# Kernel optimization log

Measured on AMD Instinct MI355X. Metric: run time of the kernel, lower is better.

The kernel has to match this reference:

```python
import jax, jax.numpy as jnp
import numpy as np

ALPHA = 0.25
GAMMA = 2.0
W_CLASS = W_BBOX = W_GIOU = W_MASK = W_DICE = W_PROJ = 1.0
EPS = 1e-8


def box_cxcywh_to_xyxy(b):
    cx, cy, w, h = jnp.split(b, 4, axis=-1)
    return jnp.concatenate([cx - 0.5 * w, cy - 0.5 * h, cx + 0.5 * w, cy + 0.5 * h], axis=-1)


def dice_coef(inputs, targets):
    # inputs: logits [N, D]; targets: binary [M, D]
    s = jax.nn.sigmoid(inputs)
    num = 2.0 * jnp.einsum('nd,md->nm', s, targets)
    den = s.sum(-1)[:, None] + targets.sum(-1)[None, :]
    return (num + 1.0) / (den + 1.0)  # [N, M]


def sigmoid_focal_coef(inputs, targets):
    # inputs: logits [N, D]; targets: binary [M, D] -> [N, M]
    x = inputs[:, None, :]
    t = targets[None, :, :]
    p = jax.nn.sigmoid(x)
    # BCE-with-logits, numerically stable
    ce = jnp.maximum(x, 0.0) - x * t + jnp.log1p(jnp.exp(-jnp.abs(x)))
    p_t = p * t + (1.0 - p) * (1.0 - t)
    alpha_t = ALPHA * t + (1.0 - ALPHA) * (1.0 - t)
    return (alpha_t * ce * (1.0 - p_t) ** GAMMA).mean(-1)


def giou_cost(src_xyxy, tgt_xyxy):
    # src [nf, nq, 4], tgt [nf, 1, 4] -> cost [nf, nq, 1]
    a1 = (src_xyxy[..., 2] - src_xyxy[..., 0]) * (src_xyxy[..., 3] - src_xyxy[..., 1])
    a2 = (tgt_xyxy[..., 2] - tgt_xyxy[..., 0]) * (tgt_xyxy[..., 3] - tgt_xyxy[..., 1])
    lt = jnp.maximum(src_xyxy[:, :, None, :2], tgt_xyxy[:, None, :, :2])
    rb = jnp.minimum(src_xyxy[:, :, None, 2:], tgt_xyxy[:, None, :, 2:])
    wh = jnp.clip(rb - lt, 0.0)
    inter = wh[..., 0] * wh[..., 1]
    union = a1[:, :, None] + a2[:, None, :] - inter
    iou = inter / union
    ltc = jnp.minimum(src_xyxy[:, :, None, :2], tgt_xyxy[:, None, :, :2])
    rbc = jnp.maximum(src_xyxy[:, :, None, 2:], tgt_xyxy[:, None, :, 2:])
    whc = jnp.clip(rbc - ltc, 0.0)
    areac = whc[..., 0] * whc[..., 1]
    giou = iou - (areac - union) / areac
    return -giou


def cost_matrix_one(logits, boxes, masks, tmask, tbox, tvalid):
    # logits [nf,nq,1], boxes [nf,nq,4], masks [nf,nq,H,W], tmask [nf,H,W], tbox [nf,4], tvalid [nf]
    p = jax.nn.sigmoid(logits[..., 0])  # [nf, nq]
    neg = (1.0 - ALPHA) * p ** GAMMA * (-jnp.log(1.0 - p + EPS))
    pos = ALPHA * (1.0 - p) ** GAMMA * (-jnp.log(p + EPS))
    w = (tvalid != 0).astype(p.dtype)  # valid-frame mask replaces python `continue`
    cost_class = (((pos - neg) * w[:, None]).sum(0) / w.sum())[:, None]  # [nq, 1]

    cost_bbox = jnp.abs(boxes[:, :, None, :] - tbox[:, None, None, :]).sum(-1).mean(0)  # [nq, 1]
    cost_giou = giou_cost(box_cxcywh_to_xyxy(boxes), box_cxcywh_to_xyxy(tbox[:, None, :])).mean(0)

    out_mask = jnp.transpose(masks, (1, 0, 2, 3))  # [nq, nf, H, W]
    nq = out_mask.shape[0]
    flat_src = out_mask.reshape(nq, -1)
    flat_tgt = tmask.reshape(1, -1)
    cost_mask = sigmoid_focal_coef(flat_src, flat_tgt)  # [nq, 1]
    cost_dice = -dice_coef(flat_src, flat_tgt)

    src_y = jnp.max(out_mask, axis=2, keepdims=True).reshape(nq, -1)  # [nq, nf*W]
    src_x = jnp.max(out_mask, axis=3, keepdims=True).reshape(nq, -1)  # [nq, nf*H]
    tgt_y = jnp.max(tmask[None], axis=2, keepdims=True).reshape(1, -1)
    tgt_x = jnp.max(tmask[None], axis=3, keepdims=True).reshape(1, -1)
    cost_proj = -0.5 * (dice_coef(src_y, tgt_y) + dice_coef(src_x, tgt_x))

    C = (W_CLASS * cost_class + W_BBOX * cost_bbox + W_GIOU * cost_giou
         + W_MASK * cost_mask + W_DICE * cost_dice + W_PROJ * cost_proj)
    return C  # [nq, 1]


def setup_inputs() -> dict:
    key = jax.random.key(0)
    k = jax.random.split(key, 6)
    bs, nf, nq, H, W = 2, 8, 300, 96, 96
    pred_logits = jax.random.normal(k[0], (bs, nf, nq, 1), dtype=jnp.float32)
    pred_boxes = jax.random.uniform(k[1], (bs, nf, nq, 4), dtype=jnp.float32)
    pred_masks = jax.random.normal(k[2], (bs, nf, nq, H, W), dtype=jnp.float32)
    target_masks = (jax.random.uniform(k[3], (bs, nf, H, W)) < 0.3).astype(jnp.float32)
    tgt_boxes = jax.random.uniform(k[4], (bs, nf, 4), dtype=jnp.float32)
    tgt_valid = jnp.ones((bs, nf), dtype=jnp.int32)
    valid_pad = jnp.zeros((bs, H, W), dtype=bool)
    return {"pred_logits": pred_logits, "pred_boxes": pred_boxes, "pred_masks": pred_masks,
            "target_masks": target_masks, "tgt_boxes": tgt_boxes, "tgt_valid": tgt_valid,
            "valid_pad": valid_pad}


def reference(pred_logits, pred_boxes, pred_masks, target_masks, tgt_boxes, tgt_valid, valid_pad):
    # zero out predictions over padded regions (masked_fill with valid[:, None, None])
    masks = jnp.where(valid_pad[:, None, None, :, :], 0.0, pred_masks)
    C = jax.vmap(cost_matrix_one)(pred_logits, pred_boxes, masks, target_masks, tgt_boxes, tgt_valid)
    src_ind = jnp.argmin(C, axis=1).astype(jnp.int64)  # [bs, 1]
    tgt_ind = jnp.zeros_like(src_ind)
    return C, src_ind, tgt_ind
```

## Files before the change

kernel.cpp:

```cpp
#include <hip/hip_runtime.h>
#include <math.h>

#define NF 8
#define NQ 300
#define HSZ 96
#define WSZ 96
#define HW 9216
#define DTOT 73728
#define NT 256
#define NTP 192
#define NBF 16

#define WS_TGTY 0
#define WS_TGTX 1536
#define WS_TSUM 3072
#define WS_YSUM 3088
#define WS_XSUM 3104
#define WS_TBITS 3200
#define WS_PBITS 7808
#define WS_PART  8448

__device__ __forceinline__ float sigmoid_fast(float x) {
    float e = __expf(-fabsf(x));
    float inv = __builtin_amdgcn_rcpf(1.f + e);
    return x >= 0.f ? inv : e * inv;
}

__global__ __launch_bounds__(NT)
void targets_kernel(const float* __restrict__ tm, const unsigned char* __restrict__ vpad,
                    float* __restrict__ ws) {
    int bf = blockIdx.x, t = threadIdx.x;
    int lane = t & 63, wv = t >> 6;
    __shared__ float tile[HSZ * 97];
    __shared__ float red[4][4];
    unsigned long long* tb64 = (unsigned long long*)(ws + WS_TBITS) + bf * 144;
    const float* base = tm + (size_t)bf * HW;
    float tsum = 0.f;
    #pragma unroll
    for (int it = 0; it < 36; ++it) {
        int e = it * NT + t;
        float v = base[e];
        tsum += v;
        unsigned long long bt = __ballot(v != 0.f);
        if (lane == 0) tb64[it * 4 + wv] = bt;
        tile[e + e / 96] = v;
    }
    if ((bf & 7) == 0) {
        int b = bf >> 3;
        unsigned long long* pb64 = (unsigned long long*)(ws + WS_PBITS) + b * 144;
        const unsigned char* pp = vpad + (size_t)b * HW;
        #pragma unroll
        for (int it = 0; it < 36; ++it) {
            int e = it * NT + t;
            unsigned long long bt = __ballot(pp[e] != 0);
            if (lane == 0) pb64[it * 4 + wv] = bt;
        }
    }
    __syncthreads();
    float ysum = 0.f, xsum = 0.f;
    if (t < 96) {
        float m = -INFINITY;
        #pragma unroll 8
        for (int h = 0; h < HSZ; ++h) m = fmaxf(m, tile[h * 97 + t]);
        ws[WS_TGTY + bf * 96 + t] = m;
        ysum = m;
    } else if (t < 192) {
        int hh = t - 96;
        float m = -INFINITY;
        #pragma unroll 8
        for (int w = 0; w < WSZ; ++w) m = fmaxf(m, tile[hh * 97 + w]);
        ws[WS_TGTX + bf * 96 + hh] = m;
        xsum = m;
    }
    float v0 = tsum, v1 = ysum, v2 = xsum;
    #pragma unroll
    for (int off = 32; off > 0; off >>= 1) {
        v0 += __shfl_down(v0, off, 64);
        v1 += __shfl_down(v1, off, 64);
        v2 += __shfl_down(v2, off, 64);
    }
    if (lane == 0) { red[wv][0] = v0; red[wv][1] = v1; red[wv][2] = v2; }
    __syncthreads();
    if (t == 0) {
        #pragma unroll
        for (int w = 1; w < 4; ++w) { v0 += red[w][0]; v1 += red[w][1]; v2 += red[w][2]; }
        ws[WS_TSUM + bf] = v0;
        ws[WS_YSUM + bf] = v1;
        ws[WS_XSUM + bf] = v2;
    }
}

__global__ __launch_bounds__(NTP, 6)
void partial_kernel(const float* __restrict__ masks, const float* __restrict__ ws,
                    float* __restrict__ part) {
    int blk = blockIdx.x;
    int bf = blk / NQ;
    int q  = blk - bf * NQ;
    int b  = bf >> 3;
    int t  = threadIdx.x;
    int w4 = t % 24;
    int g  = t / 24;

    __shared__ float rowp[HSZ * 25];
    __shared__ float colp[8 * HSZ];
    __shared__ float red[3][8];

    const float4* mrow = (const float4*)(masks + (size_t)(bf * NQ + q) * HW);
    const unsigned* tb = (const unsigned*)(ws + WS_TBITS) + bf * 288;
    const unsigned* pb = (const unsigned*)(ws + WS_PBITS) + b * 288;

    int widx = t >> 3;
    int sh = (t & 7) * 4;

    float focal = 0.f, dnum = 0.f, dden = 0.f;
    float cm0 = -INFINITY, cm1 = -INFINITY, cm2 = -INFINITY, cm3 = -INFINITY;

    #pragma unroll 3
    for (int k = 0; k < 12; ++k) {
        float4 cur = mrow[k * NTP + t];
        unsigned twc = tb[k * 24 + widx] >> sh;
        unsigned pwc = pb[k * 24 + widx] >> sh;

        float xs[4] = {cur.x, cur.y, cur.z, cur.w};
        if (pwc & 0xFu) {
            #pragma unroll
            for (int j = 0; j < 4; ++j)
                if ((pwc >> j) & 1u) xs[j] = 0.f;
        }
        #pragma unroll
        for (int j = 0; j < 4; ++j) {
            float x = xs[j];
            bool bit = (twc >> j) & 1u;
            float ee = __expf(-fabsf(x));
            float se = 1.f + ee;
            float inv = __builtin_amdgcn_rcpf(se);
            bool pos = x >= 0.f;
            float s   = pos ? inv : ee * inv;
            float oms = pos ? ee * inv : inv;
            float L = __logf(se);
            float rp = fmaxf(x, 0.f);
            float ce = (bit ? rp - x : rp) + L;
            float omp = bit ? oms : s;
            float at = bit ? 0.25f : 0.75f;
            focal = fmaf(at * ce, omp * omp, focal);
            dnum += bit ? s : 0.f;
            dden += s;
        }
        cm0 = fmaxf(cm0, xs[0]); cm1 = fmaxf(cm1, xs[1]);
        cm2 = fmaxf(cm2, xs[2]); cm3 = fmaxf(cm3, xs[3]);
        float rm = fmaxf(fmaxf(xs[0], xs[1]), fmaxf(xs[2], xs[3]));
        rowp[(g + 8 * k) * 25 + w4] = rm;
    }
    ((float4*)colp)[g * 24 + w4] = make_float4(cm0, cm1, cm2, cm3);
    __syncthreads();

    float pYn = 0.f, pYd = 0.f, pXn = 0.f, pXd = 0.f;
    if (t < 96) {
        float m = colp[t];
        #pragma unroll
        for (int gg = 1; gg < 8; ++gg) m = fmaxf(m, colp[gg * 96 + t]);
        float sg = sigmoid_fast(m);
        pYd = sg;
        pYn = sg * ws[WS_TGTY + bf * 96 + t];
    } else {
        int r = t - 96;
        float m = rowp[r * 25];
        #pragma unroll
        for (int w = 1; w < 24; ++w) m = fmaxf(m, rowp[r * 25 + w]);
        float sg = sigmoid_fast(m);
        pXd = sg;
        pXn = sg * ws[WS_TGTX + bf * 96 + r];
    }

    float v[7] = {focal, dnum, dden, pYn, pYd, pXn, pXd};
    #pragma unroll
    for (int k = 0; k < 7; ++k)
        #pragma unroll
        for (int off = 32; off > 0; off >>= 1) v[k] += __shfl_down(v[k], off, 64);
    int wv = t >> 6, lane = t & 63;
    if (lane == 0) {
        #pragma unroll
        for (int k = 0; k < 7; ++k) red[wv][k] = v[k];
    }
    __syncthreads();
    if (t == 0) {
        #pragma unroll
        for (int w = 1; w < 3; ++w)
            #pragma unroll
            for (int k = 0; k < 7; ++k) v[k] += red[w][k];
        float4* p = (float4*)(part + (size_t)blk * 8);
        p[0] = make_float4(v[0], v[1], v[2], v[3]);
        p[1] = make_float4(v[4], v[5], v[6], 0.f);
    }
}

__global__ __launch_bounds__(NT)
void final_kernel(const float* __restrict__ logits, const float* __restrict__ boxes,
                  const float* __restrict__ tbox, const int* __restrict__ tvalid,
                  const float* __restrict__ ws, float* __restrict__ out, int write_idx) {
    int b = blockIdx.x, t = threadIdx.x;
    const float* part = ws + WS_PART;

    float best = INFINITY;
    int bi = 0x7fffffff;

    for (int q = t; q < NQ; q += NT) {
        float focal = 0.f, dnum = 0.f, dden = 0.f;
        float pYn = 0.f, pYd = 0.f, pXn = 0.f, pXd = 0.f;
        float tsum = 0.f, ysum = 0.f, xsum = 0.f;
        #pragma unroll
        for (int f = 0; f < NF; ++f) {
            int bf = b * NF + f;
            const float4* p = (const float4*)(part + (size_t)(bf * NQ + q) * 8);
            float4 pa = p[0], pbv = p[1];
            focal += pa.x; dnum += pa.y; dden += pa.z; pYn += pa.w;
            pYd += pbv.x; pXn += pbv.y; pXd += pbv.z;
            tsum += ws[WS_TSUM + bf];
            ysum += ws[WS_YSUM + bf];
            xsum += ws[WS_XSUM + bf];
        }
        float cost_mask = focal / (float)DTOT;
        float cost_dice = -(2.f * dnum + 1.f) / (dden + tsum + 1.f);
        float coefY = (2.f * pYn + 1.f) / (pYd + ysum + 1.f);
        float coefX = (2.f * pXn + 1.f) / (pXd + xsum + 1.f);
        float cost_proj = -0.5f * (coefY + coefX);

        float wsum = 0.f, cls = 0.f, cb = 0.f, cg = 0.f;
        #pragma unroll
        for (int f = 0; f < NF; ++f) {
            float wv = (tvalid[b * NF + f] != 0) ? 1.f : 0.f;
            wsum += wv;
            float lg = logits[(b * NF + f) * NQ + q];
            float p = sigmoid_fast(lg);
            float negc = 0.75f * p * p * (-__logf(1.f - p + 1e-8f));
            float posc = 0.25f * (1.f - p) * (1.f - p) * (-__logf(p + 1e-8f));
            cls += (posc - negc) * wv;

            const float* bx = boxes + (size_t)((b * NF + f) * NQ + q) * 4;
            const float* tbp = tbox + (b * NF + f) * 4;
            float cx = bx[0], cy = bx[1], bw = bx[2], bh = bx[3];
            float tcx = tbp[0], tcy = tbp[1], tbw = tbp[2], tbh = tbp[3];
            cb += fabsf(cx - tcx) + fabsf(cy - tcy) + fabsf(bw - tbw) + fabsf(bh - tbh);
            float sx1 = cx - 0.5f * bw, sy1 = cy - 0.5f * bh;
            float sx2 = cx + 0.5f * bw, sy2 = cy + 0.5f * bh;
            float tx1 = tcx - 0.5f * tbw, ty1 = tcy - 0.5f * tbh;
            float tx2 = tcx + 0.5f * tbw, ty2 = tcy + 0.5f * tbh;
            float a1 = (sx2 - sx1) * (sy2 - sy1), a2 = (tx2 - tx1) * (ty2 - ty1);
            float iw = fmaxf(fminf(sx2, tx2) - fmaxf(sx1, tx1), 0.f);
            float ih = fmaxf(fminf(sy2, ty2) - fmaxf(sy1, ty1), 0.f);
            float inter = iw * ih;
            float uni = a1 + a2 - inter;
            float iou = inter / uni;
            float cw = fmaxf(fmaxf(sx2, tx2) - fminf(sx1, tx1), 0.f);
            float chh = fmaxf(fmaxf(sy2, ty2) - fminf(sy1, ty1), 0.f);
            float areac = cw * chh;
            cg += -(iou - (areac - uni) / areac);
        }
        cls /= wsum;
        float c = cls + 0.125f * cb + 0.125f * cg + cost_mask + cost_dice + cost_proj;
        out[b * NQ + q] = c;
        if (c < best) { best = c; bi = q; }
    }

    #pragma unroll
    for (int off = 32; off > 0; off >>= 1) {
        float ov = __shfl_down(best, off, 64);
        int oi = __shfl_down(bi, off, 64);
        if (ov < best || (ov == best && oi < bi)) { best = ov; bi = oi; }
    }
    __shared__ float rv[4];
    __shared__ int ri[4];
    int wv = t >> 6, lane = t & 63;
    if (lane == 0) { rv[wv] = best; ri[wv] = bi; }
    __syncthreads();
    if (t == 0 && write_idx) {
        #pragma unroll
        for (int w = 1; w < 4; ++w) {
            if (rv[w] < best || (rv[w] == best && ri[w] < bi)) { best = rv[w]; bi = ri[w]; }
        }
        out[2 * NQ + b] = (float)bi;
        out[2 * NQ + 2 + b] = 0.f;
    }
}

extern "C" void kernel_launch(void* const* d_in, const int* in_sizes, int n_in,
                              void* d_out, int out_size, void* d_ws, size_t ws_size,
                              hipStream_t stream) {
    const float* logits = (const float*)d_in[0];
    const float* boxes  = (const float*)d_in[1];
    const float* masks  = (const float*)d_in[2];
    const float* tmask  = (const float*)d_in[3];
    const float* tbox   = (const float*)d_in[4];
    const int*   tvalid = (const int*)d_in[5];
    const unsigned char* vpad = (const unsigned char*)d_in[6];
    float* out = (float*)d_out;
    float* ws  = (float*)d_ws;

    targets_kernel<<<NBF, NT, 0, stream>>>(tmask, vpad, ws);
    partial_kernel<<<NBF * NQ, NTP, 0, stream>>>(masks, ws, ws + WS_PART);
    int write_idx = (out_size >= 2 * NQ + 4) ? 1 : 0;
    final_kernel<<<2, NT, 0, stream>>>(logits, boxes, tbox, tvalid, ws, out, write_idx);
}
```

Before: 322.3 us.

## Pre-pack per-thread mask bits and split final kernel into parallel combine plus argmin

```diff
diff --git a/kernel.cpp b/kernel.cpp
--- a/kernel.cpp
+++ b/kernel.cpp
@@ -16,9 +16,11 @@
 #define WS_TSUM 3072
 #define WS_YSUM 3088
 #define WS_XSUM 3104
-#define WS_TBITS 3200
-#define WS_PBITS 7808
-#define WS_PART  8448
+#define WS_TBT  3200
+#define WS_PBT  9344
+#define WS_PART 10240
+
+typedef unsigned long long u64;
 
 __device__ __forceinline__ float sigmoid_fast(float x) {
     float e = __expf(-fabsf(x));
@@ -32,8 +34,9 @@
     int bf = blockIdx.x, t = threadIdx.x;
     int lane = t & 63, wv = t >> 6;
     __shared__ float tile[HSZ * 97];
+    __shared__ unsigned bits_t[288];
+    __shared__ unsigned bits_p[288];
     __shared__ float red[4][4];
-    unsigned long long* tb64 = (unsigned long long*)(ws + WS_TBITS) + bf * 144;
     const float* base = tm + (size_t)bf * HW;
     float tsum = 0.f;
     #pragma unroll
@@ -41,22 +44,43 @@
         int e = it * NT + t;
         float v = base[e];
         tsum += v;
-        unsigned long long bt = __ballot(v != 0.f);
-        if (lane == 0) tb64[it * 4 + wv] = bt;
+        u64 bt = __ballot(v != 0.f);
+        if (lane == 0) ((u64*)bits_t)[it * 4 + wv] = bt;
         tile[e + e / 96] = v;
     }
     if ((bf & 7) == 0) {
         int b = bf >> 3;
-        unsigned long long* pb64 = (unsigned long long*)(ws + WS_PBITS) + b * 144;
         const unsigned char* pp = vpad + (size_t)b * HW;
         #pragma unroll
         for (int it = 0; it < 36; ++it) {
             int e = it * NT + t;
-            unsigned long long bt = __ballot(pp[e] != 0);
-            if (lane == 0) pb64[it * 4 + wv] = bt;
-        }
-    }
-    __syncthreads();
+            u64 bt = __ballot(pp[e] != 0);
+            if (lane == 0) ((u64*)bits_p)[it * 4 + wv] = bt;
+        }
+    }
+    __syncthreads();
+
+    if (t < NTP) {
+        int widx = t >> 3, sh = (t & 7) * 4;
+        u64 v = 0;
+        #pragma unroll
+        for (int k = 0; k < 12; ++k) {
+            unsigned nib = (bits_t[k * 24 + widx] >> sh) & 0xFu;
+            v |= (u64)nib << (4 * k);
+        }
+        ((u64*)(ws + WS_TBT))[bf * NTP + t] = v;
+        if ((bf & 7) == 0) {
+            int b = bf >> 3;
+            u64 p = 0;
+            #pragma unroll
+            for (int k = 0; k < 12; ++k) {
+                unsigned nib = (bits_p[k * 24 + widx] >> sh) & 0xFu;
+                p |= (u64)nib << (4 * k);
+            }
+            ((u64*)(ws + WS_PBT))[b * NTP + t] = p;
+        }
+    }
+
     float ysum = 0.f, xsum = 0.f;
     if (t < 96) {
         float m = -INFINITY;
@@ -90,7 +114,7 @@
     }
 }
 
-__global__ __launch_bounds__(NTP, 6)
+__global__ __launch_bounds__(NTP, 8)
 void partial_kernel(const float* __restrict__ masks, const float* __restrict__ ws,
                     float* __restrict__ part) {
     int blk = blockIdx.x;
@@ -106,11 +130,8 @@
     __shared__ float red[3][8];
 
     const float4* mrow = (const float4*)(masks + (size_t)(bf * NQ + q) * HW);
-    const unsigned* tb = (const unsigned*)(ws + WS_TBITS) + bf * 288;
-    const unsigned* pb = (const unsigned*)(ws + WS_PBITS) + b * 288;
-
-    int widx = t >> 3;
-    int sh = (t & 7) * 4;
+    const u64 tw64 = ((const u64*)(ws + WS_TBT))[bf * NTP + t];
+    const u64 pw64 = ((const u64*)(ws + WS_PBT))[b * NTP + t];
 
     float focal = 0.f, dnum = 0.f, dden = 0.f;
     float cm0 = -INFINITY, cm1 = -INFINITY, cm2 = -INFINITY, cm3 = -INFINITY;
@@ -118,19 +139,19 @@
     #pragma unroll 3
     for (int k = 0; k < 12; ++k) {
         float4 cur = mrow[k * NTP + t];
-        unsigned twc = tb[k * 24 + widx] >> sh;
-        unsigned pwc = pb[k * 24 + widx] >> sh;
+        unsigned tn = (unsigned)(tw64 >> (4 * k)) & 0xFu;
+        unsigned pn = (unsigned)(pw64 >> (4 * k)) & 0xFu;
 
         float xs[4] = {cur.x, cur.y, cur.z, cur.w};
-        if (pwc & 0xFu) {
+        if (pn) {
             #pragma unroll
             for (int j = 0; j < 4; ++j)
-                if ((pwc >> j) & 1u) xs[j] = 0.f;
+                if ((pn >> j) & 1u) xs[j] = 0.f;
         }
         #pragma unroll
         for (int j = 0; j < 4; ++j) {
             float x = xs[j];
-            bool bit = (twc >> j) & 1u;
+            bool bit = (tn >> j) & 1u;
             float ee = __expf(-fabsf(x));
             float se = 1.f + ee;
             float inv = __builtin_amdgcn_rcpf(se);
@@ -194,74 +215,79 @@
     }
 }
 
+__global__ __launch_bounds__(64)
+void combine_kernel(const float* __restrict__ logits, const float* __restrict__ boxes,
+                    const float* __restrict__ tbox, const int* __restrict__ tvalid,
+                    const float* __restrict__ ws, float* __restrict__ out) {
+    int gid = blockIdx.x * 64 + threadIdx.x;
+    if (gid >= 2 * NQ) return;
+    int b = gid / NQ, q = gid - b * NQ;
+    const float* part = ws + WS_PART;
+
+    float focal = 0.f, dnum = 0.f, dden = 0.f;
+    float pYn = 0.f, pYd = 0.f, pXn = 0.f, pXd = 0.f;
+    float tsum = 0.f, ysum = 0.f, xsum = 0.f;
+    #pragma unroll
+    for (int f = 0; f < NF; ++f) {
+        int bf = b * NF + f;
+        const float4* p = (const float4*)(part + (size_t)(bf * NQ + q) * 8);
+        float4 pa = p[0], pbv = p[1];
+        focal += pa.x; dnum += pa.y; dden += pa.z; pYn += pa.w;
+        pYd += pbv.x; pXn += pbv.y; pXd += pbv.z;
+        tsum += ws[WS_TSUM + bf];
+        ysum += ws[WS_YSUM + bf];
+        xsum += ws[WS_XSUM + bf];
+    }
+    float cost_mask = focal / (float)DTOT;
+    float cost_dice = -(2.f * dnum + 1.f) / (dden + tsum + 1.f);
+    float coefY = (2.f * pYn + 1.f) / (pYd + ysum + 1.f);
+    float coefX = (2.f * pXn + 1.f) / (pXd + xsum + 1.f);
+    float cost_proj = -0.5f * (coefY + coefX);
+
+    float wsum = 0.f, cls = 0.f, cb = 0.f, cg = 0.f;
+    #pragma unroll
+    for (int f = 0; f < NF; ++f) {
+        float wv = (tvalid[b * NF + f] != 0) ? 1.f : 0.f;
+        wsum += wv;
+        float lg = logits[(b * NF + f) * NQ + q];
+        float p = sigmoid_fast(lg);
+        float negc = 0.75f * p * p * (-__logf(1.f - p + 1e-8f));
+        float posc = 0.25f * (1.f - p) * (1.f - p) * (-__logf(p + 1e-8f));
+        cls += (posc - negc) * wv;
+
+        const float* bx = boxes + (size_t)((b * NF + f) * NQ + q) * 4;
+        const float* tbp = tbox + (b * NF + f) * 4;
+        float cx = bx[0], cy = bx[1], bw = bx[2], bh = bx[3];
+        float tcx = tbp[0], tcy = tbp[1], tbw = tbp[2], tbh = tbp[3];
+        cb += fabsf(cx - tcx) + fabsf(cy - tcy) + fabsf(bw - tbw) + fabsf(bh - tbh);
+        float sx1 = cx - 0.5f * bw, sy1 = cy - 0.5f * bh;
+        float sx2 = cx + 0.5f * bw, sy2 = cy + 0.5f * bh;
+        float tx1 = tcx - 0.5f * tbw, ty1 = tcy - 0.5f * tbh;
+        float tx2 = tcx + 0.5f * tbw, ty2 = tcy + 0.5f * tbh;
+        float a1 = (sx2 - sx1) * (sy2 - sy1), a2 = (tx2 - tx1) * (ty2 - ty1);
+        float iw = fmaxf(fminf(sx2, tx2) - fmaxf(sx1, tx1), 0.f);
+        float ih = fmaxf(fminf(sy2, ty2) - fmaxf(sy1, ty1), 0.f);
+        float inter = iw * ih;
+        float uni = a1 + a2 - inter;
+        float iou = inter / uni;
+        float cw = fmaxf(fmaxf(sx2, tx2) - fminf(sx1, tx1), 0.f);
+        float chh = fmaxf(fmaxf(sy2, ty2) - fminf(sy1, ty1), 0.f);
+        float areac = cw * chh;
+        cg += -(iou - (areac - uni) / areac);
+    }
+    cls /= wsum;
+    out[b * NQ + q] = cls + 0.125f * cb + 0.125f * cg + cost_mask + cost_dice + cost_proj;
+}
+
 __global__ __launch_bounds__(NT)
-void final_kernel(const float* __restrict__ logits, const float* __restrict__ boxes,
-                  const float* __restrict__ tbox, const int* __restrict__ tvalid,
-                  const float* __restrict__ ws, float* __restrict__ out, int write_idx) {
+void argmin_kernel(float* __restrict__ out, int write_idx) {
     int b = blockIdx.x, t = threadIdx.x;
-    const float* part = ws + WS_PART;
-
     float best = INFINITY;
     int bi = 0x7fffffff;
-
     for (int q = t; q < NQ; q += NT) {
-        float focal = 0.f, dnum = 0.f, dden = 0.f;
-        float pYn = 0.f, pYd = 0.f, pXn = 0.f, pXd = 0.f;
-        float tsum = 0.f, ysum = 0.f, xsum = 0.f;
-        #pragma unroll
-        for (int f = 0; f < NF; ++f) {
-            int bf = b * NF + f;
-            const float4* p = (const float4*)(part + (size_t)(bf * NQ + q) * 8);
-            float4 pa = p[0], pbv = p[1];
-            focal += pa.x; dnum += pa.y; dden += pa.z; pYn += pa.w;
-            pYd += pbv.x; pXn += pbv.y; pXd += pbv.z;
-            tsum += ws[WS_TSUM + bf];
-            ysum += ws[WS_YSUM + bf];
-            xsum += ws[WS_XSUM + bf];
-        }
-        float cost_mask = focal / (float)DTOT;
-        float cost_dice = -(2.f * dnum + 1.f) / (dden + tsum + 1.f);
-        float coefY = (2.f * pYn + 1.f) / (pYd + ysum + 1.f);
-        float coefX = (2.f * pXn + 1.f) / (pXd + xsum + 1.f);
-        float cost_proj = -0.5f * (coefY + coefX);
-
-        float wsum = 0.f, cls = 0.f, cb = 0.f, cg = 0.f;
-        #pragma unroll
-        for (int f = 0; f < NF; ++f) {
-            float wv = (tvalid[b * NF + f] != 0) ? 1.f : 0.f;
-            wsum += wv;
-            float lg = logits[(b * NF + f) * NQ + q];
-            float p = sigmoid_fast(lg);
-            float negc = 0.75f * p * p * (-__logf(1.f - p + 1e-8f));
-            float posc = 0.25f * (1.f - p) * (1.f - p) * (-__logf(p + 1e-8f));
-            cls += (posc - negc) * wv;
-
-            const float* bx = boxes + (size_t)((b * NF + f) * NQ + q) * 4;
-            const float* tbp = tbox + (b * NF + f) * 4;
-            float cx = bx[0], cy = bx[1], bw = bx[2], bh = bx[3];
-            float tcx = tbp[0], tcy = tbp[1], tbw = tbp[2], tbh = tbp[3];
-            cb += fabsf(cx - tcx) + fabsf(cy - tcy) + fabsf(bw - tbw) + fabsf(bh - tbh);
-            float sx1 = cx - 0.5f * bw, sy1 = cy - 0.5f * bh;
-            float sx2 = cx + 0.5f * bw, sy2 = cy + 0.5f * bh;
-            float tx1 = tcx - 0.5f * tbw, ty1 = tcy - 0.5f * tbh;
-            float tx2 = tcx + 0.5f * tbw, ty2 = tcy + 0.5f * tbh;
-            float a1 = (sx2 - sx1) * (sy2 - sy1), a2 = (tx2 - tx1) * (ty2 - ty1);
-            float iw = fmaxf(fminf(sx2, tx2) - fmaxf(sx1, tx1), 0.f);
-            float ih = fmaxf(fminf(sy2, ty2) - fmaxf(sy1, ty1), 0.f);
-            float inter = iw * ih;
-            float uni = a1 + a2 - inter;
-            float iou = inter / uni;
-            float cw = fmaxf(fmaxf(sx2, tx2) - fminf(sx1, tx1), 0.f);
-            float chh = fmaxf(fmaxf(sy2, ty2) - fminf(sy1, ty1), 0.f);
-            float areac = cw * chh;
-            cg += -(iou - (areac - uni) / areac);
-        }
-        cls /= wsum;
-        float c = cls + 0.125f * cb + 0.125f * cg + cost_mask + cost_dice + cost_proj;
-        out[b * NQ + q] = c;
-        if (c < best) { best = c; bi = q; }
-    }
-
+        float v = out[b * NQ + q];
+        if (v < best) { best = v; bi = q; }
+    }
     #pragma unroll
     for (int off = 32; off > 0; off >>= 1) {
         float ov = __shfl_down(best, off, 64);
@@ -298,6 +324,7 @@
 
     targets_kernel<<<NBF, NT, 0, stream>>>(tmask, vpad, ws);
     partial_kernel<<<NBF * NQ, NTP, 0, stream>>>(masks, ws, ws + WS_PART);
+    combine_kernel<<<(2 * NQ + 63) / 64, 64, 0, stream>>>(logits, boxes, tbox, tvalid, ws, out);
     int write_idx = (out_size >= 2 * NQ + 4) ? 1 : 0;
-    final_kernel<<<2, NT, 0, stream>>>(logits, boxes, tbox, tvalid, ws, out, write_idx);
-}
+    argmin_kernel<<<2, NT, 0, stream>>>(out, write_idx);
+}
```

Measured after the change: 314.1 us. 2.5% less time.
